# Optimization experiments

Measured on AMD Instinct MI355X. Metric: run time of the kernel, lower is better.

## Reference

```python
import jax, jax.numpy as jnp
import numpy as np

N_SRC, N_DST, E = 100000, 50000, 1000000
IN_F, H, D = 256, 4, 32
NEG_SLOPE = 0.2


def setup_inputs() -> dict:
    key = jax.random.key(0)
    k = jax.random.split(key, 7)
    x = jax.random.normal(k[0], (N_SRC, IN_F), dtype=jnp.float32)
    # scale weights so exp() of attention logits stays well-conditioned
    fc_w = jax.random.normal(k[1], (H * D, IN_F), dtype=jnp.float32) * (1.0 / np.sqrt(IN_F))
    attn_l = jax.random.normal(k[2], (1, H, D), dtype=jnp.float32) * 0.1
    attn_r = jax.random.normal(k[3], (1, H, D), dtype=jnp.float32) * 0.1
    src_idx = jax.random.randint(k[4], (E,), 0, N_SRC, dtype=jnp.int32)
    dst_idx = jax.random.randint(k[5], (E,), 0, N_DST, dtype=jnp.int32)
    dst_node_ids = jax.random.randint(k[6], (N_DST,), 0, N_SRC, dtype=jnp.int32)
    return {"x": x, "fc_w": fc_w, "attn_l": attn_l, "attn_r": attn_r,
            "src_idx": src_idx, "dst_idx": dst_idx, "dst_node_ids": dst_node_ids}


def reference(x, fc_w, attn_l, attn_r, src_idx, dst_idx, dst_node_ids):
    # fc: [N_src, in] @ [in, H*D] -> [N_src, H, D]
    h = (x @ fc_w.T).reshape(-1, H, D)
    # per-node, per-head attention scalars
    el = jnp.einsum('nhd,ohd->nh', h, attn_l)            # [N_src, H]
    h_dst = h[dst_node_ids]                               # self_gather -> [N_dst, H, D]
    er = jnp.einsum('nhd,ohd->nh', h_dst, attn_r)        # [N_dst, H]
    # apply_edge: e = el[src] + er[dst], then leaky_relu + exp (edge softmax numerator)
    e = el[src_idx] + er[dst_idx]                         # [E, H]
    e = jnp.where(e >= 0, e, NEG_SLOPE * e)
    exp_e = jnp.exp(e)
    # apply_node: segment-sum denominators over destination nodes
    sum_exp = jax.ops.segment_sum(exp_e, dst_idx, num_segments=N_DST)  # [N_dst, H]
    att = exp_e / sum_exp[dst_idx]                        # [E, H]
    # attention_gather: weighted scatter-add of source features to dst nodes
    msg = att[:, :, None] * h[src_idx]                    # [E, H, D]
    out = jax.ops.segment_sum(msg, dst_idx, num_segments=N_DST)        # [N_dst, H, D]
    return out.reshape(N_DST, H * D)
```

## Files before the change

### kernel.cpp

```cpp
#include <hip/hip_runtime.h>
#include <hip/hip_bf16.h>

#define N_SRC_N  100000
#define N_DST_N  50000
#define NE       1000000
#define IN_F     256
#define NH       4
#define ND       32
#define HD       128
#define NEG_SLOPE 0.2f

#define DPB      32
#define NB       1563
#define CAP      1024

typedef __attribute__((ext_vector_type(8))) short short8v;
typedef __attribute__((ext_vector_type(4))) short short4v;
typedef __attribute__((ext_vector_type(4))) float f32x4;

__device__ __forceinline__ short f2bf(float f) {
    __hip_bfloat16 h = __float2bfloat16(f);
    return *reinterpret_cast<short*>(&h);
}
__device__ __forceinline__ float bflo(unsigned u) { return __uint_as_float(u << 16); }
__device__ __forceinline__ float bfhi(unsigned u) { return __uint_as_float(u & 0xffff0000u); }

__global__ __launch_bounds__(256) void cvt_w(const float* __restrict__ w,
                                             short* __restrict__ wb)
{
    int i4 = blockIdx.x * 256 + threadIdx.x;
    if (i4 < (HD * IN_F) / 4) {
        f32x4 v = ((const f32x4*)w)[i4];
        short4v s;
        s[0] = f2bf(v[0]); s[1] = f2bf(v[1]); s[2] = f2bf(v[2]); s[3] = f2bf(v[3]);
        ((short4v*)wb)[i4] = s;
    }
}

__global__ __launch_bounds__(512, 4) void gemm_fc_mfma(
    const float* __restrict__ x, const short* __restrict__ wb,
    const float* __restrict__ al, short* __restrict__ hb,
    float* __restrict__ el, const int4* __restrict__ dst4,
    int* __restrict__ bcnt)
{
    __shared__ short wlds[HD * IN_F];

    const int tid = threadIdx.x;
    {
        int row = tid >> 2, qt = tid & 3;
#pragma unroll
        for (int c = 0; c < 8; ++c) {
            int chunk = qt * 8 + c;
            short8v v = *(const short8v*)(wb + row * IN_F + chunk * 8);
            int boff = (chunk * 16) ^ ((row & 7) << 4);
            *(short8v*)((char*)wlds + row * 512 + boff) = v;
        }
    }
    __syncthreads();

    const int w  = tid >> 6;
    const int l  = tid & 63;
    const int lr = l & 15;
    const int lk = l >> 4;

    float alv[8];
#pragma unroll
    for (int ct = 0; ct < 8; ++ct) alv[ct] = al[ct * 16 + lr];

    const int wave_id = blockIdx.x * 8 + w;
    for (int tile = wave_id; tile < N_SRC_N / 16; tile += 4096) {
        const int row0 = tile * 16;
        const float* xp = x + (size_t)(row0 + lr) * IN_F + lk * 8;

        f32x4 a[16];
#pragma unroll
        for (int kk = 0; kk < 8; ++kk) {
            a[2 * kk]     = *(const f32x4*)(xp + kk * 32);
            a[2 * kk + 1] = *(const f32x4*)(xp + kk * 32 + 4);
        }
        __builtin_amdgcn_sched_barrier(0);

        f32x4 acc[8];
#pragma unroll
        for (int ct = 0; ct < 8; ++ct) acc[ct] = (f32x4){0.f, 0.f, 0.f, 0.f};

#pragma unroll
        for (int kk = 0; kk < 8; ++kk) {
            f32x4 u0 = a[2 * kk], u1 = a[2 * kk + 1];
            short8v af;
            af[0] = f2bf(u0[0]); af[1] = f2bf(u0[1]);
            af[2] = f2bf(u0[2]); af[3] = f2bf(u0[3]);
            af[4] = f2bf(u1[0]); af[5] = f2bf(u1[1]);
            af[6] = f2bf(u1[2]); af[7] = f2bf(u1[3]);
            const int boff = (kk * 64 + lk * 16) ^ ((lr & 7) << 4);
#pragma unroll
            for (int ct = 0; ct < 8; ++ct) {
                short8v bf = *(const short8v*)((const char*)wlds
                                               + (ct * 16 + lr) * 512 + boff);
                acc[ct] = __builtin_amdgcn_mfma_f32_16x16x32_bf16(af, bf, acc[ct], 0, 0, 0);
            }
        }

#pragma unroll
        for (int r = 0; r < 4; ++r) {
            short* hp = hb + (size_t)(row0 + lk * 4 + r) * HD + lr;
#pragma unroll
            for (int ct = 0; ct < 8; ++ct) hp[ct * 16] = f2bf(acc[ct][r]);
        }

#pragma unroll
        for (int h = 0; h < 4; ++h) {
            float p[4];
#pragma unroll
            for (int r = 0; r < 4; ++r)
                p[r] = acc[2 * h][r] * alv[2 * h] + acc[2 * h + 1][r] * alv[2 * h + 1];
#pragma unroll
            for (int o = 1; o < 16; o <<= 1) {
#pragma unroll
                for (int r = 0; r < 4; ++r) p[r] += __shfl_xor(p[r], o, 64);
            }
            if (lr == 0) {
#pragma unroll
                for (int r = 0; r < 4; ++r)
                    el[(row0 + lk * 4 + r) * NH + h] = p[r];
            }
        }
    }

    __syncthreads();
    int* lhist = (int*)wlds;
    for (int i = tid; i < NB; i += 512) lhist[i] = 0;
    __syncthreads();
    int e4 = blockIdx.x * 512 + tid;
    if (e4 < NE / 4) {
        int4 v = dst4[e4];
        atomicAdd(&lhist[v.x >> 5], 1); atomicAdd(&lhist[v.y >> 5], 1);
        atomicAdd(&lhist[v.z >> 5], 1); atomicAdd(&lhist[v.w >> 5], 1);
    }
    __syncthreads();
    for (int i = tid; i < NB; i += 512) {
        int c = lhist[i];
        if (c > 0) atomicAdd(&bcnt[i], c);
    }
}

__global__ __launch_bounds__(1024) void bucket_scan(
    const int* __restrict__ bcnt, int* __restrict__ boff, int* __restrict__ bcur, int n)
{
    int tid = threadIdx.x;
    int i0 = 2 * tid, i1 = 2 * tid + 1;
    int a = (i0 < n) ? bcnt[i0] : 0;
    int c = (i1 < n) ? bcnt[i1] : 0;
    int s = a + c, v = s;
#pragma unroll
    for (int o = 1; o < 64; o <<= 1) {
        int t = __shfl_up(v, o, 64);
        if ((tid & 63) >= o) v += t;
    }
    __shared__ int ws[16];
    if ((tid & 63) == 63) ws[tid >> 6] = v;
    __syncthreads();
    int add = 0;
    for (int q = 0; q < (tid >> 6); ++q) add += ws[q];
    int excl = v - s + add;
    if (i0 < n) { boff[i0] = excl;     bcur[i0] = excl; }
    if (i1 < n) { boff[i1] = excl + a; bcur[i1] = excl + a; }
}

__global__ __launch_bounds__(256) void partition(
    const int4* __restrict__ src4, const int4* __restrict__ dst4,
    int* __restrict__ bcur, int* __restrict__ ebuf, int n4)
{
    __shared__ int lh[NB];
    __shared__ int base[NB];
    for (int i = threadIdx.x; i < NB; i += 256) lh[i] = 0;
    __syncthreads();
    int4 sv[8], dv[8];
#pragma unroll
    for (int q = 0; q < 8; ++q) {
        int e4 = blockIdx.x * 2048 + q * 256 + threadIdx.x;
        if (e4 < n4) {
            sv[q] = src4[e4]; dv[q] = dst4[e4];
            atomicAdd(&lh[dv[q].x >> 5], 1); atomicAdd(&lh[dv[q].y >> 5], 1);
            atomicAdd(&lh[dv[q].z >> 5], 1); atomicAdd(&lh[dv[q].w >> 5], 1);
        } else {
            dv[q].x = -1;
        }
    }
    __syncthreads();
    for (int i = threadIdx.x; i < NB; i += 256) {
        int cnt = lh[i];
        base[i] = (cnt > 0) ? atomicAdd(&bcur[i], cnt) : 0;
        lh[i] = 0;
    }
    __syncthreads();
#pragma unroll
    for (int q = 0; q < 8; ++q) {
        if (dv[q].x < 0) continue;
        int ss[4] = {sv[q].x, sv[q].y, sv[q].z, sv[q].w};
        int dd[4] = {dv[q].x, dv[q].y, dv[q].z, dv[q].w};
#pragma unroll
        for (int j = 0; j < 4; ++j) {
            int b = dd[j] >> 5;
            int off = atomicAdd(&lh[b], 1);
            ebuf[base[b] + off] = ss[j] | ((dd[j] & 31) << 17);
        }
    }
}

__global__ __launch_bounds__(256) void gat_gather(
    const short* __restrict__ hb, const float* __restrict__ el,
    const float* __restrict__ ar, const int* __restrict__ dnid,
    const int* __restrict__ ebuf, const int* __restrict__ bcnt,
    const int* __restrict__ boff, float* __restrict__ out, int ndst)
{
    __shared__ int stage_[CAP];
    __shared__ int ssrc[CAP];
    __shared__ int lh[DPB];
    __shared__ int loff[DPB + 1];
    __shared__ int curs[DPB];

    const int b = blockIdx.x;
    const int tid = threadIdx.x;
    const int cnt = bcnt[b];
    const int gbase = boff[b];
    const int lcnt = (cnt < CAP) ? cnt : CAP;

    if (tid < DPB) lh[tid] = 0;
    __syncthreads();
    for (int i = tid; i < lcnt; i += 256) {
        int p = ebuf[gbase + i];
        stage_[i] = p;
        atomicAdd(&lh[(p >> 17) & 31], 1);
    }
    __syncthreads();
    if (tid < DPB) {
        int v = lh[tid];
#pragma unroll
        for (int o = 1; o < 32; o <<= 1) {
            int t = __shfl_up(v, o, 64);
            if (tid >= o) v += t;
        }
        loff[tid + 1] = v;
        if (tid == 0) loff[0] = 0;
    }
    __syncthreads();
    if (tid < DPB) curs[tid] = loff[tid];
    __syncthreads();
    for (int i = tid; i < lcnt; i += 256) {
        int p = stage_[i];
        int dl = (p >> 17) & 31;
        int pos = atomicAdd(&curs[dl], 1);
        ssrc[pos] = (p & 0x1FFFF) << 8;
    }
    __syncthreads();

    const int wv = tid >> 6;
    const int l  = tid & 63;
    const int head = l >> 4;
    const char* hbase = (const char*)hb + 4 * l;
    const char* ebase = (const char*)el + head * 4;
    const float ar0 = ar[2 * l], ar1 = ar[2 * l + 1];

    for (int dl = wv; dl < DPB; dl += 4) {
        int d = b * DPB + dl;
        if (d >= ndst) continue;
        int j0 = loff[dl], j1 = loff[dl + 1];

        int nid = dnid[d];
        unsigned ue = *(const unsigned*)(hbase + (size_t)nid * 256);
        float erv = bflo(ue) * ar0 + bfhi(ue) * ar1;
#pragma unroll
        for (int o = 1; o < 16; o <<= 1) erv += __shfl_xor(erv, o, 64);

        float sumA = 0.f, sumB = 0.f;
        float acc0A = 0.f, acc1A = 0.f, acc0B = 0.f, acc1B = 0.f;
        int j = j0;
        for (; j + 8 <= j1; j += 8) {
            int off[8]; unsigned u[8]; float ev[8];
#pragma unroll
            for (int q = 0; q < 8; ++q) off[q] = ssrc[j + q];
#pragma unroll
            for (int q = 0; q < 8; ++q)
                u[q] = *(const unsigned*)(hbase + off[q]);
#pragma unroll
            for (int q = 0; q < 8; ++q)
                ev[q] = *(const float*)(ebase + (off[q] >> 4));
#pragma unroll
            for (int q = 0; q < 8; ++q) {
                float e = ev[q] + erv;
                e = fmaxf(e, NEG_SLOPE * e);
                float wq = __expf(e);
                if (q & 1) {
                    sumB += wq;
                    acc0B = fmaf(wq, bflo(u[q]), acc0B);
                    acc1B = fmaf(wq, bfhi(u[q]), acc1B);
                } else {
                    sumA += wq;
                    acc0A = fmaf(wq, bflo(u[q]), acc0A);
                    acc1A = fmaf(wq, bfhi(u[q]), acc1A);
                }
            }
        }
        for (; j < j1; ++j) {
            int off0 = ssrc[j];
            unsigned u0 = *(const unsigned*)(hbase + off0);
            float e0 = *(const float*)(ebase + (off0 >> 4)) + erv;
            e0 = fmaxf(e0, NEG_SLOPE * e0);
            float w0 = __expf(e0);
            sumA += w0;
            acc0A = fmaf(w0, bflo(u0), acc0A); acc1A = fmaf(w0, bfhi(u0), acc1A);
        }
        if (cnt > CAP) {
            for (int t = CAP; t < cnt; ++t) {
                int p = ebuf[gbase + t];
                if (((p >> 17) & 31) == dl) {
                    int off0 = (p & 0x1FFFF) << 8;
                    unsigned u0 = *(const unsigned*)(hbase + off0);
                    float e0 = *(const float*)(ebase + (off0 >> 4)) + erv;
                    e0 = fmaxf(e0, NEG_SLOPE * e0);
                    float w0 = __expf(e0);
                    sumA += w0;
                    acc0A = fmaf(w0, bflo(u0), acc0A); acc1A = fmaf(w0, bfhi(u0), acc1A);
                }
            }
        }
        float sum = sumA + sumB;
        bool any = (j1 > j0) || (cnt > CAP);
        float inv = any ? 1.f / sum : 0.f;
        float2 o2 = make_float2((acc0A + acc0B) * inv, (acc1A + acc1B) * inv);
        *(float2*)(out + (size_t)d * HD + 2 * l) = o2;
    }
}

extern "C" void kernel_launch(void* const* d_in, const int* in_sizes, int n_in,
                              void* d_out, int out_size, void* d_ws, size_t ws_size,
                              hipStream_t stream)
{
    const float* x   = (const float*)d_in[0];
    const float* fw  = (const float*)d_in[1];
    const float* al  = (const float*)d_in[2];
    const float* ar  = (const float*)d_in[3];
    const int*   src = (const int*)d_in[4];
    const int*   dst = (const int*)d_in[5];
    const int*   dnid= (const int*)d_in[6];
    float* out = (float*)d_out;

    char* ws = (char*)d_ws;
    size_t off = 0;
    auto alloc = [&](size_t bytes) -> void* {
        void* p = ws + off;
        off = (off + bytes + 255) & ~(size_t)255;
        return p;
    };
    short* hb   = (short*)alloc((size_t)N_SRC_N * HD * sizeof(short));
    short* wb   = (short*)alloc((size_t)HD * IN_F * sizeof(short));
    float* el   = (float*)alloc((size_t)N_SRC_N * NH * sizeof(float));
    int*   ebuf = (int*)alloc((size_t)NE * sizeof(int));
    int*   bcnt = (int*)alloc((size_t)NB * sizeof(int));
    int*   boff = (int*)alloc((size_t)NB * sizeof(int));
    int*   bcur = (int*)alloc((size_t)NB * sizeof(int));

    hipMemsetAsync(bcnt, 0, (size_t)NB * sizeof(int), stream);

    cvt_w<<<(HD * IN_F / 4 + 255) / 256, 256, 0, stream>>>(fw, wb);
    gemm_fc_mfma<<<512, 512, 0, stream>>>(x, wb, al, hb, el, (const int4*)dst, bcnt);
    bucket_scan<<<1, 1024, 0, stream>>>(bcnt, boff, bcur, NB);
    partition<<<(NE / 4 + 2047) / 2048, 256, 0, stream>>>((const int4*)src, (const int4*)dst,
                                                          bcur, ebuf, NE / 4);
    gat_gather<<<NB, 256, 0, stream>>>(hb, el, ar, dnid, ebuf, bcnt, boff, out, N_DST_N);
}
```

Baseline: 125.0 us.

## Double-buffer x tile loads in FC GEMM with fewer waves per block

The FC GEMM kernel now runs 256-thread blocks (4 waves, 2048 waves in total) and processes two tiles per loop iteration. It keeps two register buffers so the global loads for the next tile are issued before computing the current one. The goal is to hide global-memory latency for x behind MFMA work, at the cost of doubled A-register usage and half as many resident waves. The dst histogram pass is changed to a strided loop so 256-thread blocks still cover every edge.

After: 121.2 us (median of 2 runs). 3.1% less time.

```diff
diff --git a/kernel.cpp b/kernel.cpp
--- a/kernel.cpp
+++ b/kernel.cpp
@@ -14,6 +14,9 @@
 #define NB       1563
 #define CAP      1024
 
+#define NTILE    (N_SRC_N / 16)
+#define NWAVES   2048
+
 typedef __attribute__((ext_vector_type(8))) short short8v;
 typedef __attribute__((ext_vector_type(4))) short short4v;
 typedef __attribute__((ext_vector_type(4))) float f32x4;
@@ -37,7 +40,7 @@
     }
 }
 
-__global__ __launch_bounds__(512, 4) void gemm_fc_mfma(
+__global__ __launch_bounds__(256, 2) void gemm_fc_mfma(
     const float* __restrict__ x, const short* __restrict__ wb,
     const float* __restrict__ al, short* __restrict__ hb,
     float* __restrict__ el, const int4* __restrict__ dst4,
@@ -47,10 +50,10 @@
 
     const int tid = threadIdx.x;
     {
-        int row = tid >> 2, qt = tid & 3;
-#pragma unroll
-        for (int c = 0; c < 8; ++c) {
-            int chunk = qt * 8 + c;
+        int row = tid >> 1, half = tid & 1;
+#pragma unroll
+        for (int c = 0; c < 16; ++c) {
+            int chunk = half * 16 + c;
             short8v v = *(const short8v*)(wb + row * IN_F + chunk * 8);
             int boff = (chunk * 16) ^ ((row & 7) << 4);
             *(short8v*)((char*)wlds + row * 512 + boff) = v;
@@ -67,23 +70,24 @@
 #pragma unroll
     for (int ct = 0; ct < 8; ++ct) alv[ct] = al[ct * 16 + lr];
 
-    const int wave_id = blockIdx.x * 8 + w;
-    for (int tile = wave_id; tile < N_SRC_N / 16; tile += 4096) {
+    const int wave_id = blockIdx.x * 4 + w;
+
+    f32x4 aA[16], aB[16];
+
+    auto LOADA = [&](f32x4 (&dst)[16], int tile) {
+        const float* xp = x + (size_t)(tile * 16 + lr) * IN_F + lk * 8;
+#pragma unroll
+        for (int kk = 0; kk < 8; ++kk) {
+            dst[2 * kk]     = *(const f32x4*)(xp + kk * 32);
+            dst[2 * kk + 1] = *(const f32x4*)(xp + kk * 32 + 4);
+        }
+    };
+
+    auto COMPUTE = [&](f32x4 (&a)[16], int tile) {
         const int row0 = tile * 16;
-        const float* xp = x + (size_t)(row0 + lr) * IN_F + lk * 8;
-
-        f32x4 a[16];
-#pragma unroll
-        for (int kk = 0; kk < 8; ++kk) {
-            a[2 * kk]     = *(const f32x4*)(xp + kk * 32);
-            a[2 * kk + 1] = *(const f32x4*)(xp + kk * 32 + 4);
-        }
-        __builtin_amdgcn_sched_barrier(0);
-
         f32x4 acc[8];
 #pragma unroll
         for (int ct = 0; ct < 8; ++ct) acc[ct] = (f32x4){0.f, 0.f, 0.f, 0.f};
-
 #pragma unroll
         for (int kk = 0; kk < 8; ++kk) {
             f32x4 u0 = a[2 * kk], u1 = a[2 * kk + 1];
@@ -100,14 +104,12 @@
                 acc[ct] = __builtin_amdgcn_mfma_f32_16x16x32_bf16(af, bf, acc[ct], 0, 0, 0);
             }
         }
-
 #pragma unroll
         for (int r = 0; r < 4; ++r) {
             short* hp = hb + (size_t)(row0 + lk * 4 + r) * HD + lr;
 #pragma unroll
             for (int ct = 0; ct < 8; ++ct) hp[ct * 16] = f2bf(acc[ct][r]);
         }
-
 #pragma unroll
         for (int h = 0; h < 4; ++h) {
             float p[4];
@@ -125,20 +127,31 @@
                     el[(row0 + lk * 4 + r) * NH + h] = p[r];
             }
         }
+    };
+
+    if (wave_id < NTILE) LOADA(aA, wave_id);
+    for (int t = wave_id; t < NTILE; t += 2 * NWAVES) {
+        int tB = t + NWAVES;
+        if (tB < NTILE) LOADA(aB, tB);
+        __builtin_amdgcn_sched_barrier(0);
+        COMPUTE(aA, t);
+        int tA2 = t + 2 * NWAVES;
+        if (tA2 < NTILE) LOADA(aA, tA2);
+        __builtin_amdgcn_sched_barrier(0);
+        if (tB < NTILE) COMPUTE(aB, tB);
     }
 
     __syncthreads();
     int* lhist = (int*)wlds;
-    for (int i = tid; i < NB; i += 512) lhist[i] = 0;
-    __syncthreads();
-    int e4 = blockIdx.x * 512 + tid;
-    if (e4 < NE / 4) {
+    for (int i = tid; i < NB; i += 256) lhist[i] = 0;
+    __syncthreads();
+    for (int e4 = blockIdx.x * 256 + tid; e4 < NE / 4; e4 += 512 * 256) {
         int4 v = dst4[e4];
         atomicAdd(&lhist[v.x >> 5], 1); atomicAdd(&lhist[v.y >> 5], 1);
         atomicAdd(&lhist[v.z >> 5], 1); atomicAdd(&lhist[v.w >> 5], 1);
     }
     __syncthreads();
-    for (int i = tid; i < NB; i += 512) {
+    for (int i = tid; i < NB; i += 256) {
         int c = lhist[i];
         if (c > 0) atomicAdd(&bcnt[i], c);
     }
@@ -364,7 +377,7 @@
     hipMemsetAsync(bcnt, 0, (size_t)NB * sizeof(int), stream);
 
     cvt_w<<<(HD * IN_F / 4 + 255) / 256, 256, 0, stream>>>(fw, wb);
-    gemm_fc_mfma<<<512, 512, 0, stream>>>(x, wb, al, hb, el, (const int4*)dst, bcnt);
+    gemm_fc_mfma<<<512, 256, 0, stream>>>(x, wb, al, hb, el, (const int4*)dst, bcnt);
     bucket_scan<<<1, 1024, 0, stream>>>(bcnt, boff, bcur, NB);
     partition<<<(NE / 4 + 2047) / 2048, 256, 0, stream>>>((const int4*)src, (const int4*)dst,
                                                           bcur, ebuf, NE / 4);
```
